# Kernel optimization log

Hardware: AMD Instinct MI355X
Metric: run time of the kernel (lower is better)

Reference implementation:

```python
import jax, jax.numpy as jnp
import numpy as np

H = 512        # hidden_dim
D_IN = 512     # input_dim
N_ACT = 16     # output_dim
DICT = 8192    # dict_len (episodic memory slots)
B = 4096       # batch
N_CYCLES = 10  # LCA iterations
DT_T = 0.6     # LCA dt/tau
EPS = 1e-8     # cosine-similarity eps


def setup_inputs() -> dict:
    key = jax.random.key(0)
    ks = jax.random.split(key, 12)
    NHT = 4 * H + 3  # (N_VSIG+1)*H + N_SSIG
    s = lambda i, shape, sc=1.0: jax.random.normal(ks[i], shape, jnp.float32) * sc
    return {
        "x_t": s(0, (1, B, D_IN)),
        "h_prev": s(1, (1, B, H), 0.1),
        "c_prev": s(2, (1, B, H), 0.1),
        "W_i2h": s(3, (NHT, D_IN), 1.0 / np.sqrt(D_IN)),
        "b_i2h": jnp.zeros((NHT,), jnp.float32),
        "W_h2h": s(4, (NHT, H), 1.0 / np.sqrt(H)),
        "b_h2h": jnp.zeros((NHT,), jnp.float32),
        "vals": s(5, (DICT, H), 0.1),  # episodic memory table
        "W_ih": s(6, (H, H), 1.0 / np.sqrt(H)),
        "b_ih": jnp.zeros((H,), jnp.float32),
        "W_actor": s(7, (N_ACT, H), 1.0 / np.sqrt(H)),
        "b_actor": jnp.zeros((N_ACT,), jnp.float32),
        "W_critic": s(8, (1, H), 1.0 / np.sqrt(H)),
        "b_critic": jnp.zeros((1,), jnp.float32),
        "mem_ptr": 0,
    }


def _lca(sim, leak, comp, w_input):
    # Leaky competing accumulator over memory slots; sim:[B,DICT], scalars:[B,1]
    ff = w_input * sim
    def step(V, _):
        inhib = comp * (jnp.sum(V, axis=-1, keepdims=True) - V)  # lateral inhibition (excl. self)
        V = jax.nn.relu(V + DT_T * (ff - leak * V - inhib))
        return V, None
    V, _ = jax.lax.scan(step, jnp.zeros_like(sim), None, length=N_CYCLES)
    return V


def reference(x_t, h_prev, c_prev, W_i2h, b_i2h, W_h2h, b_h2h, vals,
              W_ih, b_ih, W_actor, b_actor, W_critic, b_critic, mem_ptr):
    x, h, c = x_t[0], h_prev[0], c_prev[0]  # [B, dim]
    preact = x @ W_i2h.T + b_i2h + h @ W_h2h.T + b_h2h  # [B, 4H+3]
    gates = jax.nn.sigmoid(preact[:, :3 * H])
    f_t = gates[:, :H]
    o_t = gates[:, H:2 * H]
    i_t = gates[:, 2 * H:3 * H]
    inps = jax.nn.sigmoid(preact[:, 3 * H + 0])[:, None]  # input strength (gain=1)
    leak = jax.nn.sigmoid(preact[:, 3 * H + 1])[:, None]
    comp = jax.nn.sigmoid(preact[:, 3 * H + 2])[:, None]
    c_new = jnp.tanh(preact[:, 3 * H + 3:])
    c_t = c * f_t + i_t * c_new
    # --- recall: cosine similarity vs memory, then LCA competition ---
    qn = jnp.linalg.norm(c_t, axis=-1, keepdims=True)        # [B,1]
    mn = jnp.linalg.norm(vals, axis=-1, keepdims=True)       # [DICT,1]
    sim = (c_t @ vals.T) / jnp.maximum(qn * mn.T, EPS)       # [B,DICT]
    w = _lca(sim, leak, comp, inps)                          # [B,DICT]
    m_t = w @ vals                                           # [B,H]
    cm_t = c_t + m_t
    # --- encode: ring-buffer scatter write of cm_t into memory ---
    idx = (mem_ptr + jnp.arange(B)) % DICT
    new_vals = vals.at[idx].set(cm_t)
    h_t = o_t * jnp.tanh(cm_t)
    # --- A2C head ---
    a2c_h = jax.nn.relu(h_t @ W_ih.T + b_ih)
    pi = jax.nn.softmax(a2c_h @ W_actor.T + b_actor, axis=-1)
    value = a2c_h @ W_critic.T + b_critic
    return pi, value, h_t, cm_t, m_t, new_vals
```

## Files before the change

### kernel.cpp

```cpp
#include <hip/hip_runtime.h>
#include <hip/hip_fp16.h>
#include <math.h>

#define HH    512
#define NHT   2051
#define PRE_LD 2176
#define DICT  8192
#define BATCH 4096
#define NCYC  10
#define DTT   0.6f

#define BM  128
#define BKT 64

using f16x8 = __attribute__((ext_vector_type(8))) _Float16;
using f32x4 = __attribute__((ext_vector_type(4))) float;

__device__ __forceinline__ float sigmoidf_(float x) { return 1.0f / (1.0f + __expf(-x)); }

__device__ __forceinline__ float waveReduceSum(float v) {
#pragma unroll
  for (int o = 1; o < 64; o <<= 1) v += __shfl_xor(v, o);
  return v;
}

__device__ __forceinline__ void gld16(const void* g, void* l) {
  __builtin_amdgcn_global_load_lds(
      (const __attribute__((address_space(1))) void*)g,
      (__attribute__((address_space(3))) void*)l, 16, 0, 0);
}

template<int ROWS>
__device__ __forceinline__ void stage_tile(const __half* gbase, int ld, char* lds, int tid) {
  constexpr int ISS = ROWS * 8 / 256;
#pragma unroll
  for (int i = 0; i < ISS; ++i) {
    int cidx = i * 256 + tid;
    int row  = cidx >> 3;
    int slot = cidx & 7;
    int k4   = slot ^ (row & 7);
    gld16(gbase + (size_t)row * ld + k4 * 8, lds + cidx * 16);
  }
}

__device__ __forceinline__ f16x8 frag_ld(const char* lds, int row, int kchunk) {
  int slot = kchunk ^ (row & 7);
  return *(const f16x8*)(lds + row * 128 + slot * 16);
}

template<int FN>
__device__ __forceinline__ void tile_mfma(const char* As, const char* Bs,
                                          int lane, int wr, int wc, f32x4 (&acc)[4][FN]) {
  const int g = lane >> 4, r = lane & 15;
#pragma unroll
  for (int ks = 0; ks < 2; ++ks) {
    f16x8 af[4], bfr[FN];
#pragma unroll
    for (int i = 0; i < 4; ++i)
      af[i] = frag_ld(As, wr * 64 + i * 16 + r, ks * 4 + g);
#pragma unroll
    for (int j = 0; j < FN; ++j)
      bfr[j] = frag_ld(Bs, wc * (FN * 16) + j * 16 + r, ks * 4 + g);
#pragma unroll
    for (int i = 0; i < 4; ++i)
#pragma unroll
      for (int j = 0; j < FN; ++j)
        acc[i][j] = __builtin_amdgcn_mfma_f32_16x16x32_f16(af[i], bfr[j], acc[i][j], 0, 0, 0);
  }
}

template<int BN, int FN>
__device__ __forceinline__ void gemm_seg(const __half* A, int lda, const __half* B, int ldb,
                                         int m0, int n0, int K, char* lds, int tid,
                                         f32x4 (&acc)[4][FN]) {
  constexpr int ABYTES = BM * BKT * 2;
  constexpr int BBYTES = BN * BKT * 2;
  const int lane = tid & 63, wid = tid >> 6;
  const int wr = wid >> 1, wc = wid & 1;
  const int nt = K / BKT;
  const __half* Ab = A + (size_t)m0 * lda;
  const __half* Bb = B + (size_t)n0 * ldb;
  stage_tile<BM>(Ab, lda, lds, tid);
  stage_tile<BN>(Bb, ldb, lds + ABYTES, tid);
  __syncthreads();
  int cur = 0;
  for (int t = 0; t < nt - 1; ++t) {
    char* nxt = lds + (cur ^ 1) * (ABYTES + BBYTES);
    stage_tile<BM>(Ab + (t + 1) * BKT, lda, nxt, tid);
    stage_tile<BN>(Bb + (t + 1) * BKT, ldb, nxt + ABYTES, tid);
    char* curb = lds + cur * (ABYTES + BBYTES);
    tile_mfma<FN>(curb, curb + ABYTES, lane, wr, wc, acc);
    __syncthreads();
    cur ^= 1;
  }
  char* curb = lds + cur * (ABYTES + BBYTES);
  tile_mfma<FN>(curb, curb + ABYTES, lane, wr, wc, acc);
  __syncthreads();
}

__device__ __forceinline__ void zero_acc4(f32x4 (&a)[4][4]) {
  f32x4 z = {0.f, 0.f, 0.f, 0.f};
#pragma unroll
  for (int i = 0; i < 4; ++i)
#pragma unroll
    for (int j = 0; j < 4; ++j) a[i][j] = z;
}
__device__ __forceinline__ void zero_acc2(f32x4 (&a)[4][2]) {
  f32x4 z = {0.f, 0.f, 0.f, 0.f};
#pragma unroll
  for (int i = 0; i < 4; ++i)
#pragma unroll
    for (int j = 0; j < 2; ++j) a[i][j] = z;
}

__global__ __launch_bounds__(256) void k_prep_cvt(
    const float* __restrict__ x, const float* __restrict__ h,
    const float* __restrict__ Wi, const float* __restrict__ Wh, const float* __restrict__ Wih,
    __half* __restrict__ x_h, __half* __restrict__ h_h,
    __half* __restrict__ Wi_h, __half* __restrict__ Wh_h, __half* __restrict__ Wih_h) {
  int gq = blockIdx.x * 256 + threadIdx.x;
  const float* src; __half* dst; int iq; int nin;
  if      (gq < 524288)  { src = x;   dst = x_h;   iq = gq;           nin = 2097152; }
  else if (gq < 1048576) { src = h;   dst = h_h;   iq = gq - 524288;  nin = 2097152; }
  else if (gq < 1327104) { src = Wi;  dst = Wi_h;  iq = gq - 1048576; nin = 1050112; }
  else if (gq < 1605632) { src = Wh;  dst = Wh_h;  iq = gq - 1327104; nin = 1050112; }
  else if (gq < 1671168) { src = Wih; dst = Wih_h; iq = gq - 1605632; nin = 262144;  }
  else return;
  int i = iq * 4;
  float4 v;
  if (i + 3 < nin) v = *(const float4*)(src + i);
  else v = make_float4(i + 0 < nin ? src[i + 0] : 0.f, i + 1 < nin ? src[i + 1] : 0.f,
                       i + 2 < nin ? src[i + 2] : 0.f, i + 3 < nin ? src[i + 3] : 0.f);
  *(__half2*)(dst + i)     = __floats2half2_rn(v.x, v.y);
  *(__half2*)(dst + i + 2) = __floats2half2_rn(v.z, v.w);
}

__global__ __launch_bounds__(256) void k_prep_vals(
    const float* __restrict__ vals, float* __restrict__ nv,
    __half* __restrict__ vals_h, float* __restrict__ rmn) {
  const int row  = blockIdx.x * 4 + (threadIdx.x >> 6);
  const int lane = threadIdx.x & 63;
  const float* vr = vals + (size_t)row * HH + lane * 8;
  float4 a = *(const float4*)(vr);
  float4 b = *(const float4*)(vr + 4);
  float* nvp = nv + (size_t)row * HH + lane * 8;
  *(float4*)(nvp)     = a;
  *(float4*)(nvp + 4) = b;
  __half* vh = vals_h + (size_t)row * HH + lane * 8;
  *(__half2*)(vh)     = __floats2half2_rn(a.x, a.y);
  *(__half2*)(vh + 2) = __floats2half2_rn(a.z, a.w);
  *(__half2*)(vh + 4) = __floats2half2_rn(b.x, b.y);
  *(__half2*)(vh + 6) = __floats2half2_rn(b.z, b.w);
  float ss = a.x * a.x + a.y * a.y + a.z * a.z + a.w * a.w
           + b.x * b.x + b.y * b.y + b.z * b.z + b.w * b.w;
  ss = waveReduceSum(ss);
  if (lane == 0) rmn[row] = 1.f / fmaxf(sqrtf(ss), 1e-12f);
}

__global__ __launch_bounds__(256) void k_tr(const float* __restrict__ vals, __half* __restrict__ vT) {
  __shared__ float tile[32][33];
  int r0 = blockIdx.x * 32, c0 = blockIdx.y * 32;
  int tr = threadIdx.x >> 5, tc = threadIdx.x & 31;
#pragma unroll
  for (int p = 0; p < 4; ++p)
    tile[tr + p * 8][tc] = vals[(size_t)(r0 + tr + p * 8) * HH + c0 + tc];
  __syncthreads();
#pragma unroll
  for (int p = 0; p < 4; ++p)
    vT[(size_t)(c0 + tr + p * 8) * DICT + r0 + tc] = __float2half(tile[tc][tr + p * 8]);
}

__global__ __launch_bounds__(256) void k_preact(
    const __half* __restrict__ x_h, const __half* __restrict__ h_h,
    const __half* __restrict__ Wi_h, const __half* __restrict__ Wh_h,
    const float* __restrict__ bi, const float* __restrict__ bh, float* __restrict__ pre) {
  __shared__ char smem[2 * (BM * BKT * 2 + 128 * BKT * 2)] __attribute__((aligned(16)));
  const int tid = threadIdx.x;
  const int m0 = blockIdx.y * 128, n0 = blockIdx.x * 128;
  f32x4 acc[4][4]; zero_acc4(acc);
  gemm_seg<128, 4>(x_h, HH, Wi_h, HH, m0, n0, HH, smem, tid, acc);
  gemm_seg<128, 4>(h_h, HH, Wh_h, HH, m0, n0, HH, smem, tid, acc);
  const int lane = tid & 63, wid = tid >> 6, wr = wid >> 1, wc = wid & 1;
#pragma unroll
  for (int fi = 0; fi < 4; ++fi)
#pragma unroll
    for (int fj = 0; fj < 4; ++fj)
#pragma unroll
      for (int q = 0; q < 4; ++q) {
        int n = n0 + wc * 64 + fj * 16 + (lane & 15);
        if (n < NHT) {
          int m = m0 + wr * 64 + fi * 16 + (lane >> 4) * 4 + q;
          pre[(size_t)m * PRE_LD + n] = acc[fi][fj][q] + bi[n] + bh[n];
        }
      }
}

__global__ __launch_bounds__(256) void k_gates(
    const float* __restrict__ pre, const float* __restrict__ c_prev,
    const float* __restrict__ x, const float* __restrict__ h,
    const float* __restrict__ Wi, const float* __restrict__ Wh,
    const float* __restrict__ bi, const float* __restrict__ bh,
    float* __restrict__ ct, float* __restrict__ ot, __half* __restrict__ ct_h,
    float* __restrict__ inps, float* __restrict__ leak,
    float* __restrict__ comp, float* __restrict__ rqn) {
  const int b = blockIdx.x, t = threadIdx.x;
  const float* row = pre + (size_t)b * PRE_LD;
  float ss = 0.f;
#pragma unroll
  for (int j = t; j < HH; j += 256) {
    float f  = sigmoidf_(row[j]);
    float o  = sigmoidf_(row[HH + j]);
    float ii = sigmoidf_(row[2 * HH + j]);
    float cn = tanhf(row[3 * HH + 3 + j]);
    float c  = c_prev[(size_t)b * HH + j] * f + ii * cn;
    size_t off = (size_t)b * HH + j;
    ct[off] = c; ot[off] = o; ct_h[off] = __float2half(c);
    ss += c * c;
  }
  ss = waveReduceSum(ss);
  __shared__ float ps[4];
  if ((t & 63) == 0) ps[t >> 6] = ss;
  const int wid = t >> 6, lane = t & 63;
  float sg = 0.f;
  if (wid < 3) {
    const float* wi = Wi + (size_t)(3 * HH + wid) * HH;
    const float* wh = Wh + (size_t)(3 * HH + wid) * HH;
#pragma unroll
    for (int j = lane; j < HH; j += 64)
      sg += x[(size_t)b * HH + j] * wi[j] + h[(size_t)b * HH + j] * wh[j];
    sg = waveReduceSum(sg);
  }
  __syncthreads();
  if (t == 0) rqn[b] = 1.f / fmaxf(sqrtf(ps[0] + ps[1] + ps[2] + ps[3]), 1e-12f);
  if (wid < 3 && lane == 0) {
    float v = sigmoidf_(sg + bi[3 * HH + wid] + bh[3 * HH + wid]);
    if (wid == 0) inps[b] = v; else if (wid == 1) leak[b] = v; else comp[b] = v;
  }
}

__global__ __launch_bounds__(256) void k_sim(
    const __half* __restrict__ ct_h, const __half* __restrict__ vals_h,
    const float* __restrict__ rqn, const float* __restrict__ rmn, float* __restrict__ sim) {
  __shared__ char smem[2 * (BM * BKT * 2 + 128 * BKT * 2)] __attribute__((aligned(16)));
  const int tid = threadIdx.x;
  const int m0 = blockIdx.y * 128, n0 = blockIdx.x * 128;
  f32x4 acc[4][4]; zero_acc4(acc);
  gemm_seg<128, 4>(ct_h, HH, vals_h, HH, m0, n0, HH, smem, tid, acc);
  const int lane = tid & 63, wid = tid >> 6, wr = wid >> 1, wc = wid & 1;
#pragma unroll
  for (int fi = 0; fi < 4; ++fi)
#pragma unroll
    for (int fj = 0; fj < 4; ++fj)
#pragma unroll
      for (int q = 0; q < 4; ++q) {
        int m = m0 + wr * 64 + fi * 16 + (lane >> 4) * 4 + q;
        int n = n0 + wc * 64 + fj * 16 + (lane & 15);
        sim[(size_t)m * DICT + n] = acc[fi][fj][q] * rqn[m] * rmn[n];
      }
}

__global__ __launch_bounds__(256) void k_lca(
    const float* __restrict__ sim, const float* __restrict__ inps,
    const float* __restrict__ leak, const float* __restrict__ comp, __half* __restrict__ w_h) {
  const int b = blockIdx.x, t = threadIdx.x;
  const float* srow = sim + (size_t)b * DICT;
  const float ffs = DTT * inps[b];
  const float a   = 1.0f - DTT * leak[b] + DTT * comp[b];
  const float cdt = DTT * comp[b];
  float ff[32], V[32];
#pragma unroll
  for (int i = 0; i < 32; ++i) { ff[i] = ffs * srow[t + i * 256]; V[i] = 0.f; }
  __shared__ float ps[4];
  for (int it = 0; it < NCYC; ++it) {
    float s = 0.f;
#pragma unroll
    for (int i = 0; i < 32; ++i) s += V[i];
    s = waveReduceSum(s);
    if ((t & 63) == 0) ps[t >> 6] = s;
    __syncthreads();
    float S = ps[0] + ps[1] + ps[2] + ps[3];
    __syncthreads();
    float sub = cdt * S;
#pragma unroll
    for (int i = 0; i < 32; ++i) V[i] = fmaxf(fmaf(a, V[i], ff[i] - sub), 0.f);
  }
  __half* wrow = w_h + (size_t)b * DICT;
#pragma unroll
  for (int i = 0; i < 32; ++i) wrow[t + i * 256] = __float2half(V[i]);
}

__global__ __launch_bounds__(256) void k_mt_p(
    const __half* __restrict__ w_h, const __half* __restrict__ vT_h,
    float* __restrict__ partial) {
  __shared__ char smem[2 * (BM * BKT * 2 + 64 * BKT * 2)] __attribute__((aligned(16)));
  const int tid = threadIdx.x, bid = blockIdx.x;
  const int xcd = bid & 7, idx = bid >> 3;
  const int n = idx & 7, q = idx >> 3;
  const int g = (q << 3) | xcd;
  const int m = g >> 2, s = g & 3;
  const int m0 = m * 128, n0 = n * 64;
  f32x4 acc[4][2]; zero_acc2(acc);
  gemm_seg<64, 2>(w_h + s * 2048, DICT, vT_h + s * 2048, DICT, m0, n0, 2048, smem, tid, acc);
  const int lane = tid & 63, wid = tid >> 6, wr = wid >> 1, wc = wid & 1;
  float* pbase = partial + (size_t)s * (BATCH * HH);
#pragma unroll
  for (int fi = 0; fi < 4; ++fi)
#pragma unroll
    for (int fj = 0; fj < 2; ++fj)
#pragma unroll
      for (int qq = 0; qq < 4; ++qq) {
        int mm = m0 + wr * 64 + fi * 16 + (lane >> 4) * 4 + qq;
        int nn = n0 + wc * 32 + fj * 16 + (lane & 15);
        pbase[(size_t)mm * HH + nn] = acc[fi][fj][qq];
      }
}

__global__ __launch_bounds__(256) void k_mt_red(
    const float* __restrict__ partial,
    const float* __restrict__ ct, const float* __restrict__ ot, const int* __restrict__ mptr,
    float* __restrict__ out_mt, float* __restrict__ out_cmt, float* __restrict__ out_ht,
    float* __restrict__ out_nv, __half* __restrict__ ht_h) {
  const int i4 = blockIdx.x * 256 + threadIdx.x;
  const size_t off = (size_t)i4 * 4;
  const int m = i4 >> 7;
  float4 p  = *(const float4*)(partial + off);
  float4 p1 = *(const float4*)(partial + 2097152 + off);
  float4 p2 = *(const float4*)(partial + 4194304 + off);
  float4 p3 = *(const float4*)(partial + 6291456 + off);
  p.x += p1.x + p2.x + p3.x;
  p.y += p1.y + p2.y + p3.y;
  p.z += p1.z + p2.z + p3.z;
  p.w += p1.w + p2.w + p3.w;
  float4 c4 = *(const float4*)(ct + off);
  float4 o4 = *(const float4*)(ot + off);
  float4 cm, hv;
  cm.x = c4.x + p.x; hv.x = o4.x * tanhf(cm.x);
  cm.y = c4.y + p.y; hv.y = o4.y * tanhf(cm.y);
  cm.z = c4.z + p.z; hv.z = o4.z * tanhf(cm.z);
  cm.w = c4.w + p.w; hv.w = o4.w * tanhf(cm.w);
  *(float4*)(out_mt + off)  = p;
  *(float4*)(out_cmt + off) = cm;
  *(float4*)(out_ht + off)  = hv;
  *(__half2*)(ht_h + off)     = __floats2half2_rn(hv.x, hv.y);
  *(__half2*)(ht_h + off + 2) = __floats2half2_rn(hv.z, hv.w);
  const int nvrow = (mptr[0] + m) & (DICT - 1);
  *(float4*)(out_nv + (size_t)nvrow * HH + (off & 511)) = cm;
}

__global__ __launch_bounds__(256) void k_a2c(
    const __half* __restrict__ ht_h, const __half* __restrict__ Wih_h,
    const float* __restrict__ bih, float* __restrict__ a2c) {
  __shared__ char smem[2 * (BM * BKT * 2 + 64 * BKT * 2)] __attribute__((aligned(16)));
  const int tid = threadIdx.x;
  const int bid = blockIdx.x;
  const int xn = (bid >> 3) & 7, ym = (bid & 7) | ((bid >> 6) << 3);
  const int m0 = ym * 128, n0 = xn * 64;
  f32x4 acc[4][2]; zero_acc2(acc);
  gemm_seg<64, 2>(ht_h, HH, Wih_h, HH, m0, n0, HH, smem, tid, acc);
  const int lane = tid & 63, wid = tid >> 6, wr = wid >> 1, wc = wid & 1;
#pragma unroll
  for (int fi = 0; fi < 4; ++fi)
#pragma unroll
    for (int fj = 0; fj < 2; ++fj)
#pragma unroll
      for (int q = 0; q < 4; ++q) {
        int m = m0 + wr * 64 + fi * 16 + (lane >> 4) * 4 + q;
        int n = n0 + wc * 32 + fj * 16 + (lane & 15);
        a2c[(size_t)m * HH + n] = fmaxf(acc[fi][fj][q] + bih[n], 0.f);
      }
}

__global__ __launch_bounds__(256) void k_actor(
    const float* __restrict__ a2c,
    const float* __restrict__ Wact, const float* __restrict__ bact,
    const float* __restrict__ Wcr, const float* __restrict__ bcr,
    float* __restrict__ out_pi, float* __restrict__ out_val) {
  const int b = blockIdx.x * 4 + (threadIdx.x >> 6);
  const int lane = threadIdx.x & 63;
  const float* hrow = a2c + (size_t)b * HH;
  float4 a0 = *(const float4*)(hrow + (lane << 3));
  float4 a1 = *(const float4*)(hrow + (lane << 3) + 4);
  float lg[17];
#pragma unroll
  for (int o = 0; o < 17; ++o) {
    const float* wr = (o < 16) ? (Wact + (size_t)o * HH) : Wcr;
    float4 w0 = *(const float4*)(wr + (lane << 3));
    float4 w1 = *(const float4*)(wr + (lane << 3) + 4);
    float s = a0.x * w0.x + a0.y * w0.y + a0.z * w0.z + a0.w * w0.w
            + a1.x * w1.x + a1.y * w1.y + a1.z * w1.z + a1.w * w1.w;
    lg[o] = waveReduceSum(s);
  }
#pragma unroll
  for (int o = 0; o < 16; ++o) lg[o] += bact[o];
  float mx = lg[0];
#pragma unroll
  for (int o = 1; o < 16; ++o) mx = fmaxf(mx, lg[o]);
  float e[16], sum = 0.f;
#pragma unroll
  for (int o = 0; o < 16; ++o) { e[o] = __expf(lg[o] - mx); sum += e[o]; }
  float rs = 1.f / sum;
  if (lane == 0) {
#pragma unroll
    for (int o = 0; o < 16; ++o) out_pi[(size_t)b * 16 + o] = e[o] * rs;
    out_val[b] = lg[16] + bcr[0];
  }
}

extern "C" void kernel_launch(void* const* d_in, const int* in_sizes, int n_in,
                              void* d_out, int out_size, void* d_ws, size_t ws_size,
                              hipStream_t stream) {
  const float* x    = (const float*)d_in[0];
  const float* h    = (const float*)d_in[1];
  const float* c    = (const float*)d_in[2];
  const float* Wi   = (const float*)d_in[3];
  const float* bi   = (const float*)d_in[4];
  const float* Wh   = (const float*)d_in[5];
  const float* bh   = (const float*)d_in[6];
  const float* vals = (const float*)d_in[7];
  const float* Wih  = (const float*)d_in[8];
  const float* bih  = (const float*)d_in[9];
  const float* Wact = (const float*)d_in[10];
  const float* bact = (const float*)d_in[11];
  const float* Wcr  = (const float*)d_in[12];
  const float* bcr  = (const float*)d_in[13];
  const int*   mptr = (const int*)d_in[14];

  float* F = (float*)d_ws;
  float*  pre    = F;
  __half* w_h    = (__half*)F;
  float*  sim     = F + 16777216;
  float*  a2c     = sim;
  float*  partial = sim + 16777216;
  float*  ct     = F + 50331648;
  float*  ot     = F + 52428800;
  __half* ct_h   = (__half*)(F + 54525952);
  __half* vals_h = (__half*)(F + 55574528);
  __half* vT_h   = (__half*)(F + 57671680);
  __half* x_h    = (__half*)(F + 59768832);
  __half* ht_h   = x_h;
  __half* h_h    = (__half*)(F + 60817408);
  __half* Wi_h   = (__half*)(F + 61865984);
  __half* Wh_h   = (__half*)(F + 62423040);
  __half* Wih_h  = (__half*)(F + 62980096);
  float*  inps   = F + 63111168;
  float*  leak   = inps + 4096;
  float*  comp   = leak + 4096;
  float*  rqn    = comp + 4096;
  float*  rmn    = rqn + 4096;

  float* out     = (float*)d_out;
  float* out_pi  = out;
  float* out_val = out + 65536;
  float* out_ht  = out + 69632;
  float* out_cmt = out_ht + 2097152;
  float* out_mt  = out_cmt + 2097152;
  float* out_nv  = out_mt + 2097152;

  dim3 b256(256);
  k_prep_cvt <<<6528, b256, 0, stream>>>(x, h, Wi, Wh, Wih, x_h, h_h, Wi_h, Wh_h, Wih_h);
  k_prep_vals<<<2048, b256, 0, stream>>>(vals, out_nv, vals_h, rmn);
  k_tr <<<dim3(256, 16), b256, 0, stream>>>(vals, vT_h);
  k_preact<<<dim3(17, 32), b256, 0, stream>>>(x_h, h_h, Wi_h, Wh_h, bi, bh, pre);
  k_gates <<<BATCH, b256, 0, stream>>>(pre, c, x, h, Wi, Wh, bi, bh,
                                       ct, ot, ct_h, inps, leak, comp, rqn);
  k_sim   <<<dim3(64, 32), b256, 0, stream>>>(ct_h, vals_h, rqn, rmn, sim);
  k_lca   <<<BATCH, b256, 0, stream>>>(sim, inps, leak, comp, w_h);
  k_mt_p  <<<1024, b256, 0, stream>>>(w_h, vT_h, partial);
  k_mt_red<<<2048, b256, 0, stream>>>(partial, ct, ot, mptr,
                                      out_mt, out_cmt, out_ht, out_nv, ht_h);
  k_a2c   <<<256, b256, 0, stream>>>(ht_h, Wih_h, bih, a2c);
  k_actor <<<BATCH / 4, b256, 0, stream>>>(a2c, Wact, bact, Wcr, bcr, out_pi, out_val);
}
```

Baseline: 258.9 us.

## Fuse LSTM gate epilogue into preact GEMM via permuted weights; store sim in fp16

The prep kernel now permutes the gate rows of W_i2h/W_h2h so that each 64-column wave tile holds matching f/o/i/c_new columns for 16 hidden units. This lets the preact GEMM epilogue compute c_t, o_t and the fp16 copy of c_t directly, with no [B,2176] fp32 preact round trip. A small new kernel computes the three scalar gates and the query norm. The similarity matrix is stored as fp16 instead of fp32, halving its 128MB write and read, and the LCA kernel uses contiguous per-thread vector loads and stores. The cost is reduced precision on sim before the LCA and an extra kernel launch.

```diff
diff --git a/kernel.cpp b/kernel.cpp
--- a/kernel.cpp
+++ b/kernel.cpp
@@ -3,8 +3,6 @@
 #include <math.h>
 
 #define HH    512
-#define NHT   2051
-#define PRE_LD 2176
 #define DICT  8192
 #define BATCH 4096
 #define NCYC  10
@@ -117,22 +115,34 @@
     const float* __restrict__ x, const float* __restrict__ h,
     const float* __restrict__ Wi, const float* __restrict__ Wh, const float* __restrict__ Wih,
     __half* __restrict__ x_h, __half* __restrict__ h_h,
-    __half* __restrict__ Wi_h, __half* __restrict__ Wh_h, __half* __restrict__ Wih_h) {
+    __half* __restrict__ Wip_h, __half* __restrict__ Whp_h, __half* __restrict__ Wih_h) {
   int gq = blockIdx.x * 256 + threadIdx.x;
-  const float* src; __half* dst; int iq; int nin;
-  if      (gq < 524288)  { src = x;   dst = x_h;   iq = gq;           nin = 2097152; }
-  else if (gq < 1048576) { src = h;   dst = h_h;   iq = gq - 524288;  nin = 2097152; }
-  else if (gq < 1327104) { src = Wi;  dst = Wi_h;  iq = gq - 1048576; nin = 1050112; }
-  else if (gq < 1605632) { src = Wh;  dst = Wh_h;  iq = gq - 1327104; nin = 1050112; }
-  else if (gq < 1671168) { src = Wih; dst = Wih_h; iq = gq - 1605632; nin = 262144;  }
-  else return;
-  int i = iq * 4;
-  float4 v;
-  if (i + 3 < nin) v = *(const float4*)(src + i);
-  else v = make_float4(i + 0 < nin ? src[i + 0] : 0.f, i + 1 < nin ? src[i + 1] : 0.f,
-                       i + 2 < nin ? src[i + 2] : 0.f, i + 3 < nin ? src[i + 3] : 0.f);
-  *(__half2*)(dst + i)     = __floats2half2_rn(v.x, v.y);
-  *(__half2*)(dst + i + 2) = __floats2half2_rn(v.z, v.w);
+  const float* src; __half* dst; int si, di;
+  if (gq < 524288) {
+    src = x; dst = x_h; si = di = gq * 4;
+  } else if (gq < 1048576) {
+    src = h; dst = h_h; si = di = (gq - 524288) * 4;
+  } else if (gq < 1310720) {
+    int iq = gq - 1048576;
+    int jp = iq >> 7, k4 = (iq & 127) << 2;
+    int U = jp >> 6, g = (jp >> 4) & 3, r = jp & 15;
+    int u = U * 16 + r;
+    int orig = g * 512 + u + (g == 3 ? 3 : 0);
+    src = Wi; dst = Wip_h; si = orig * 512 + k4; di = jp * 512 + k4;
+  } else if (gq < 1572864) {
+    int iq = gq - 1310720;
+    int jp = iq >> 7, k4 = (iq & 127) << 2;
+    int U = jp >> 6, g = (jp >> 4) & 3, r = jp & 15;
+    int u = U * 16 + r;
+    int orig = g * 512 + u + (g == 3 ? 3 : 0);
+    src = Wh; dst = Whp_h; si = orig * 512 + k4; di = jp * 512 + k4;
+  } else if (gq < 1638400) {
+    int iq = gq - 1572864;
+    src = Wih; dst = Wih_h; si = di = iq * 4;
+  } else return;
+  float4 v = *(const float4*)(src + si);
+  *(__half2*)(dst + di)     = __floats2half2_rn(v.x, v.y);
+  *(__half2*)(dst + di + 2) = __floats2half2_rn(v.z, v.w);
 }
 
 __global__ __launch_bounds__(256) void k_prep_vals(
@@ -172,75 +182,81 @@
 
 __global__ __launch_bounds__(256) void k_preact(
     const __half* __restrict__ x_h, const __half* __restrict__ h_h,
-    const __half* __restrict__ Wi_h, const __half* __restrict__ Wh_h,
-    const float* __restrict__ bi, const float* __restrict__ bh, float* __restrict__ pre) {
+    const __half* __restrict__ Wip, const __half* __restrict__ Whp,
+    const float* __restrict__ bi, const float* __restrict__ bh,
+    const float* __restrict__ c_prev,
+    float* __restrict__ ct, float* __restrict__ ot, __half* __restrict__ ct_h) {
   __shared__ char smem[2 * (BM * BKT * 2 + 128 * BKT * 2)] __attribute__((aligned(16)));
   const int tid = threadIdx.x;
   const int m0 = blockIdx.y * 128, n0 = blockIdx.x * 128;
   f32x4 acc[4][4]; zero_acc4(acc);
-  gemm_seg<128, 4>(x_h, HH, Wi_h, HH, m0, n0, HH, smem, tid, acc);
-  gemm_seg<128, 4>(h_h, HH, Wh_h, HH, m0, n0, HH, smem, tid, acc);
+  gemm_seg<128, 4>(x_h, HH, Wip, HH, m0, n0, HH, smem, tid, acc);
+  gemm_seg<128, 4>(h_h, HH, Whp, HH, m0, n0, HH, smem, tid, acc);
   const int lane = tid & 63, wid = tid >> 6, wr = wid >> 1, wc = wid & 1;
+  const int r = lane & 15;
+  const int u = ((n0 >> 6) + wc) * 16 + r;
+  float bsum[4];
+#pragma unroll
+  for (int g = 0; g < 4; ++g) {
+    int orig = g * 512 + u + (g == 3 ? 3 : 0);
+    bsum[g] = bi[orig] + bh[orig];
+  }
 #pragma unroll
   for (int fi = 0; fi < 4; ++fi)
 #pragma unroll
-    for (int fj = 0; fj < 4; ++fj)
-#pragma unroll
-      for (int q = 0; q < 4; ++q) {
-        int n = n0 + wc * 64 + fj * 16 + (lane & 15);
-        if (n < NHT) {
-          int m = m0 + wr * 64 + fi * 16 + (lane >> 4) * 4 + q;
-          pre[(size_t)m * PRE_LD + n] = acc[fi][fj][q] + bi[n] + bh[n];
-        }
-      }
-}
-
-__global__ __launch_bounds__(256) void k_gates(
-    const float* __restrict__ pre, const float* __restrict__ c_prev,
+    for (int q = 0; q < 4; ++q) {
+      int m = m0 + wr * 64 + fi * 16 + (lane >> 4) * 4 + q;
+      float f  = sigmoidf_(acc[fi][0][q] + bsum[0]);
+      float o  = sigmoidf_(acc[fi][1][q] + bsum[1]);
+      float ii = sigmoidf_(acc[fi][2][q] + bsum[2]);
+      float cn = tanhf(acc[fi][3][q] + bsum[3]);
+      size_t off = (size_t)m * HH + u;
+      float cc = c_prev[off] * f + ii * cn;
+      ct[off] = cc; ot[off] = o; ct_h[off] = __float2half(cc);
+    }
+}
+
+__global__ __launch_bounds__(256) void k_scalars(
     const float* __restrict__ x, const float* __restrict__ h,
     const float* __restrict__ Wi, const float* __restrict__ Wh,
     const float* __restrict__ bi, const float* __restrict__ bh,
-    float* __restrict__ ct, float* __restrict__ ot, __half* __restrict__ ct_h,
+    const float* __restrict__ ct,
     float* __restrict__ inps, float* __restrict__ leak,
     float* __restrict__ comp, float* __restrict__ rqn) {
-  const int b = blockIdx.x, t = threadIdx.x;
-  const float* row = pre + (size_t)b * PRE_LD;
-  float ss = 0.f;
-#pragma unroll
-  for (int j = t; j < HH; j += 256) {
-    float f  = sigmoidf_(row[j]);
-    float o  = sigmoidf_(row[HH + j]);
-    float ii = sigmoidf_(row[2 * HH + j]);
-    float cn = tanhf(row[3 * HH + 3 + j]);
-    float c  = c_prev[(size_t)b * HH + j] * f + ii * cn;
-    size_t off = (size_t)b * HH + j;
-    ct[off] = c; ot[off] = o; ct_h[off] = __float2half(c);
-    ss += c * c;
-  }
-  ss = waveReduceSum(ss);
-  __shared__ float ps[4];
-  if ((t & 63) == 0) ps[t >> 6] = ss;
-  const int wid = t >> 6, lane = t & 63;
-  float sg = 0.f;
+  const int b = blockIdx.x, wid = threadIdx.x >> 6, lane = threadIdx.x & 63;
+  const int j = lane * 8;
   if (wid < 3) {
-    const float* wi = Wi + (size_t)(3 * HH + wid) * HH;
-    const float* wh = Wh + (size_t)(3 * HH + wid) * HH;
-#pragma unroll
-    for (int j = lane; j < HH; j += 64)
-      sg += x[(size_t)b * HH + j] * wi[j] + h[(size_t)b * HH + j] * wh[j];
-    sg = waveReduceSum(sg);
-  }
-  __syncthreads();
-  if (t == 0) rqn[b] = 1.f / fmaxf(sqrtf(ps[0] + ps[1] + ps[2] + ps[3]), 1e-12f);
-  if (wid < 3 && lane == 0) {
-    float v = sigmoidf_(sg + bi[3 * HH + wid] + bh[3 * HH + wid]);
-    if (wid == 0) inps[b] = v; else if (wid == 1) leak[b] = v; else comp[b] = v;
+    const float* wi = Wi + (size_t)(1536 + wid) * HH + j;
+    const float* wh = Wh + (size_t)(1536 + wid) * HH + j;
+    const float* xr = x + (size_t)b * HH + j;
+    const float* hr = h + (size_t)b * HH + j;
+    float4 xa = *(const float4*)(xr), xb = *(const float4*)(xr + 4);
+    float4 wa = *(const float4*)(wi), wb = *(const float4*)(wi + 4);
+    float4 ha = *(const float4*)(hr), hb = *(const float4*)(hr + 4);
+    float4 va = *(const float4*)(wh), vb = *(const float4*)(wh + 4);
+    float s = xa.x * wa.x + xa.y * wa.y + xa.z * wa.z + xa.w * wa.w
+            + xb.x * wb.x + xb.y * wb.y + xb.z * wb.z + xb.w * wb.w
+            + ha.x * va.x + ha.y * va.y + ha.z * va.z + ha.w * va.w
+            + hb.x * vb.x + hb.y * vb.y + hb.z * vb.z + hb.w * vb.w;
+    s = waveReduceSum(s);
+    if (lane == 0) {
+      float v = sigmoidf_(s + bi[1536 + wid] + bh[1536 + wid]);
+      if (wid == 0) inps[b] = v; else if (wid == 1) leak[b] = v; else comp[b] = v;
+    }
+  } else {
+    const float* cr = ct + (size_t)b * HH + j;
+    float4 a = *(const float4*)(cr), d = *(const float4*)(cr + 4);
+    float ss = a.x * a.x + a.y * a.y + a.z * a.z + a.w * a.w
+             + d.x * d.x + d.y * d.y + d.z * d.z + d.w * d.w;
+    ss = waveReduceSum(ss);
+    if (lane == 0) rqn[b] = 1.f / fmaxf(sqrtf(ss), 1e-12f);
   }
 }
 
 __global__ __launch_bounds__(256) void k_sim(
     const __half* __restrict__ ct_h, const __half* __restrict__ vals_h,
-    const float* __restrict__ rqn, const float* __restrict__ rmn, float* __restrict__ sim) {
+    const float* __restrict__ rqn, const float* __restrict__ rmn,
+    __half* __restrict__ sim_h) {
   __shared__ char smem[2 * (BM * BKT * 2 + 128 * BKT * 2)] __attribute__((aligned(16)));
   const int tid = threadIdx.x;
   const int m0 = blockIdx.y * 128, n0 = blockIdx.x * 128;
@@ -255,21 +271,26 @@
       for (int q = 0; q < 4; ++q) {
         int m = m0 + wr * 64 + fi * 16 + (lane >> 4) * 4 + q;
         int n = n0 + wc * 64 + fj * 16 + (lane & 15);
-        sim[(size_t)m * DICT + n] = acc[fi][fj][q] * rqn[m] * rmn[n];
+        sim_h[(size_t)m * DICT + n] = __float2half(acc[fi][fj][q] * rqn[m] * rmn[n]);
       }
 }
 
 __global__ __launch_bounds__(256) void k_lca(
-    const float* __restrict__ sim, const float* __restrict__ inps,
-    const float* __restrict__ leak, const float* __restrict__ comp, __half* __restrict__ w_h) {
+    const __half* __restrict__ sim_h, const float* __restrict__ inps,
+    const float* __restrict__ leak, const float* __restrict__ comp,
+    __half* __restrict__ w_h) {
   const int b = blockIdx.x, t = threadIdx.x;
-  const float* srow = sim + (size_t)b * DICT;
+  const __half* srow = sim_h + (size_t)b * DICT + t * 32;
   const float ffs = DTT * inps[b];
   const float a   = 1.0f - DTT * leak[b] + DTT * comp[b];
   const float cdt = DTT * comp[b];
   float ff[32], V[32];
 #pragma unroll
-  for (int i = 0; i < 32; ++i) { ff[i] = ffs * srow[t + i * 256]; V[i] = 0.f; }
+  for (int i = 0; i < 4; ++i) {
+    f16x8 v8 = *(const f16x8*)(srow + i * 8);
+#pragma unroll
+    for (int j = 0; j < 8; ++j) { ff[i * 8 + j] = ffs * (float)v8[j]; V[i * 8 + j] = 0.f; }
+  }
   __shared__ float ps[4];
   for (int it = 0; it < NCYC; ++it) {
     float s = 0.f;
@@ -284,9 +305,14 @@
 #pragma unroll
     for (int i = 0; i < 32; ++i) V[i] = fmaxf(fmaf(a, V[i], ff[i] - sub), 0.f);
   }
-  __half* wrow = w_h + (size_t)b * DICT;
-#pragma unroll
-  for (int i = 0; i < 32; ++i) wrow[t + i * 256] = __float2half(V[i]);
+  __half* wrow = w_h + (size_t)b * DICT + t * 32;
+#pragma unroll
+  for (int i = 0; i < 4; ++i) {
+    f16x8 o8;
+#pragma unroll
+    for (int j = 0; j < 8; ++j) o8[j] = (_Float16)V[i * 8 + j];
+    *(f16x8*)(wrow + i * 8) = o8;
+  }
 }
 
 __global__ __launch_bounds__(256) void k_mt_p(
@@ -426,11 +452,10 @@
   const int*   mptr = (const int*)d_in[14];
 
   float* F = (float*)d_ws;
-  float*  pre    = F;
   __half* w_h    = (__half*)F;
-  float*  sim     = F + 16777216;
-  float*  a2c     = sim;
-  float*  partial = sim + 16777216;
+  __half* sim_h   = (__half*)(F + 16777216);
+  float*  a2c     = F + 16777216;
+  float*  partial = F + 33554432;
   float*  ct     = F + 50331648;
   float*  ot     = F + 52428800;
   __half* ct_h   = (__half*)(F + 54525952);
@@ -439,8 +464,8 @@
   __half* x_h    = (__half*)(F + 59768832);
   __half* ht_h   = x_h;
   __half* h_h    = (__half*)(F + 60817408);
-  __half* Wi_h   = (__half*)(F + 61865984);
-  __half* Wh_h   = (__half*)(F + 62423040);
+  __half* Wip_h  = (__half*)(F + 61865984);
+  __half* Whp_h  = (__half*)(F + 62423040);
   __half* Wih_h  = (__half*)(F + 62980096);
   float*  inps   = F + 63111168;
   float*  leak   = inps + 4096;
@@ -457,17 +482,17 @@
   float* out_nv  = out_mt + 2097152;
 
   dim3 b256(256);
-  k_prep_cvt <<<6528, b256, 0, stream>>>(x, h, Wi, Wh, Wih, x_h, h_h, Wi_h, Wh_h, Wih_h);
+  k_prep_cvt <<<6400, b256, 0, stream>>>(x, h, Wi, Wh, Wih, x_h, h_h, Wip_h, Whp_h, Wih_h);
   k_prep_vals<<<2048, b256, 0, stream>>>(vals, out_nv, vals_h, rmn);
   k_tr <<<dim3(256, 16), b256, 0, stream>>>(vals, vT_h);
-  k_preact<<<dim3(17, 32), b256, 0, stream>>>(x_h, h_h, Wi_h, Wh_h, bi, bh, pre);
-  k_gates <<<BATCH, b256, 0, stream>>>(pre, c, x, h, Wi, Wh, bi, bh,
-                                       ct, ot, ct_h, inps, leak, comp, rqn);
-  k_sim   <<<dim3(64, 32), b256, 0, stream>>>(ct_h, vals_h, rqn, rmn, sim);
-  k_lca   <<<BATCH, b256, 0, stream>>>(sim, inps, leak, comp, w_h);
-  k_mt_p  <<<1024, b256, 0, stream>>>(w_h, vT_h, partial);
-  k_mt_red<<<2048, b256, 0, stream>>>(partial, ct, ot, mptr,
-                                      out_mt, out_cmt, out_ht, out_nv, ht_h);
-  k_a2c   <<<256, b256, 0, stream>>>(ht_h, Wih_h, bih, a2c);
-  k_actor <<<BATCH / 4, b256, 0, stream>>>(a2c, Wact, bact, Wcr, bcr, out_pi, out_val);
-}
+  k_preact <<<dim3(16, 32), b256, 0, stream>>>(x_h, h_h, Wip_h, Whp_h, bi, bh, c,
+                                               ct, ot, ct_h);
+  k_scalars<<<BATCH, b256, 0, stream>>>(x, h, Wi, Wh, bi, bh, ct, inps, leak, comp, rqn);
+  k_sim    <<<dim3(64, 32), b256, 0, stream>>>(ct_h, vals_h, rqn, rmn, sim_h);
+  k_lca    <<<BATCH, b256, 0, stream>>>(sim_h, inps, leak, comp, w_h);
+  k_mt_p   <<<1024, b256, 0, stream>>>(w_h, vT_h, partial);
+  k_mt_red <<<2048, b256, 0, stream>>>(partial, ct, ot, mptr,
+                                       out_mt, out_cmt, out_ht, out_nv, ht_h);
+  k_a2c    <<<256, b256, 0, stream>>>(ht_h, Wih_h, bih, a2c);
+  k_actor  <<<BATCH / 4, b256, 0, stream>>>(a2c, Wact, bact, Wcr, bcr, out_pi, out_val);
+}
```

After: 234.8 us. -9.3%, faster.
